# Kernel tuning notes

Hardware: AMD Instinct MI355X
Metric: run time of the kernel (lower is better)

The kernel has to match this reference:

```python
import math
import jax, jax.numpy as jnp
import numpy as np

B, N, D, H, PQ, PV = 2, 2048, 256, 8, 4, 8
HD = D // H
OUT_IN = D + H * PV * 3 + H  # 256 + 192 + 8 = 456


def setup_inputs() -> dict:
    key = jax.random.key(0)
    ks = jax.random.split(key, 12)
    w = lambda k, shape: (jax.random.normal(k, shape, jnp.float32) * 0.02)
    return {
        "x": jax.random.normal(ks[0], (B, N, D), jnp.float32),
        "rotations": jax.random.normal(ks[1], (B, N, 3, 3), jnp.float32),
        "translations": jax.random.normal(ks[2], (B, N, 3), jnp.float32),
        "mask": jnp.ones((B, N), dtype=bool),
        "Wq": w(ks[3], (D, D)), "bq": jnp.zeros((D,), jnp.float32),
        "Wk": w(ks[4], (D, D)), "bk": jnp.zeros((D,), jnp.float32),
        "Wv": w(ks[5], (D, D)), "bv": jnp.zeros((D,), jnp.float32),
        "Wo": w(ks[6], (OUT_IN, D)), "bo": jnp.zeros((D,), jnp.float32),
        "head_weights": jnp.ones((H,), jnp.float32),
    }


def reference(x, rotations, translations, mask, Wq, bq, Wk, bk, Wv, bv, Wo, bo, head_weights):
    b, n, d = x.shape
    h = head_weights.shape[0]
    hd = d // h
    pv3 = Wo.shape[0] - d - h  # num_heads * num_value_points * 3

    q = (x @ Wq + bq).reshape(b, n, h, hd)
    k = (x @ Wk + bk).reshape(b, n, h, hd)
    v = (x @ Wv + bv).reshape(b, n, h, hd)

    # scalar attention logits [b,h,i,j]
    attn_scores = jnp.einsum("bihd,bjhd->bhij", q, k) / math.sqrt(hd)

    # point-distance bias from frame translations (rotated q/k/v points are
    # dead code in the original module and are omitted)
    diff = translations[:, :, None, :] - translations[:, None, :, :]  # [b,i,j,3]
    dist_sq = jnp.sum(diff * diff, axis=-1)                            # [b,i,j]
    point_attn = -0.5 * dist_sq[:, None, :, :]                         # [b,1,i,j]

    weights = jax.nn.softmax(head_weights)                             # [h]
    combined = attn_scores + point_attn * weights[None, :, None, None]
    combined = jnp.where(mask[:, None, None, :], combined, -1e9)
    attn_probs = jax.nn.softmax(combined, axis=-1)                     # [b,h,i,j]

    attn_output = jnp.einsum("bhij,bjhd->bihd", attn_probs, v).reshape(b, n, d)

    # translation-weighted points, brought back to local frame
    trans_weighted = jnp.einsum("bhij,bjc->bihc", attn_probs, translations)  # [b,i,h,3]
    trans_local = trans_weighted - translations[:, :, None, :]
    point_out = trans_local.reshape(b, n, h * 3)
    point_out = jnp.pad(point_out, ((0, 0), (0, 0), (0, pv3 - h * 3)))

    mean_dist = jnp.sqrt(jnp.mean(dist_sq, axis=-1, keepdims=True) + 1e-8)  # [b,n,1]
    pair_features = jnp.broadcast_to(mean_dist, (b, n, h))

    output = jnp.concatenate([attn_output, point_out, pair_features], axis=-1)
    return output @ Wo + bo
```

## Files before the change

### kernel.cpp

```cpp
#include <hip/hip_runtime.h>

typedef unsigned short u16;
typedef __attribute__((ext_vector_type(8))) short bf16x8;
typedef __attribute__((ext_vector_type(4))) float f32x4;
typedef __attribute__((ext_vector_type(16))) float f32x16;
typedef __attribute__((ext_vector_type(4))) unsigned u32x4;

#define NB 2
#define NSEQ 2048
#define DD 256
#define NH 8
#define HD 32
#define NTOK 4096
#define KF 288
#define NSPLIT 4
#define PS 36
#define TSTR 4096

#define SCL2E 0.25506973f
#define L2E 1.4426950408889634f

__device__ __forceinline__ u16 f2b(float f) {
  unsigned u = __builtin_bit_cast(unsigned, f);
  return (u16)((u + 0x7fffu + ((u >> 16) & 1u)) >> 16);
}

__device__ __forceinline__ unsigned cvt_pk_bf16(float lo, float hi) {
  unsigned r;
  asm("v_cvt_pk_bf16_f32 %0, %1, %2" : "=v"(r) : "v"(lo), "v"(hi));
  return r;
}

__device__ __forceinline__ void permlane32_swap(unsigned& a, unsigned& b) {
  asm volatile("v_permlane32_swap_b32 %0, %1" : "+v"(a), "+v"(b));
}

__device__ __forceinline__ f32x4 mfma16(bf16x8 a, bf16x8 b, f32x4 c) {
  return __builtin_amdgcn_mfma_f32_16x16x32_bf16(a, b, c, 0, 0, 0);
}
__device__ __forceinline__ f32x16 mfma32(bf16x8 a, bf16x8 b, f32x16 c) {
  return __builtin_amdgcn_mfma_f32_32x32x16_bf16(a, b, c, 0, 0, 0);
}

#define PB0 1024
#define PB1 (PB0 + 264)
#define PB2 (PB1 + 2)
#define PB3 (PB2 + 16)
__global__ __launch_bounds__(256) void prep(
    const float* __restrict__ x, const float* __restrict__ tr,
    const float* __restrict__ hw, const float* __restrict__ bq,
    const float* __restrict__ bk, const float* __restrict__ bv,
    const float* __restrict__ Wq, const float* __restrict__ Wk,
    const float* __restrict__ Wv, const float* __restrict__ Wo,
    u16* __restrict__ xb, u16* __restrict__ WqkvT, u16* __restrict__ WoPT,
    float4* __restrict__ t4, float4* __restrict__ bstat,
    float* __restrict__ b_all, float* __restrict__ wsoft) {
  __shared__ float lt[32][33];
  const int bid = blockIdx.x, t = threadIdx.x;
  if (bid < PB0) {
    const int i4 = bid * 256 + t;
    float4 v = *(const float4*)(x + (size_t)i4 * 4);
    ushort4 o;
    o.x = f2b(v.x); o.y = f2b(v.y); o.z = f2b(v.z); o.w = f2b(v.w);
    *(ushort4*)(xb + (size_t)i4 * 4) = o;
  } else if (bid < PB1) {
    const int bw = bid - PB0;
    const int r = t >> 3, c4 = (t & 7) * 4;
    if (bw < 192) {
      int mt = bw >> 3, kt = bw & 7;
      int m0 = mt * 32, k0 = kt * 32;
      const float* W = m0 < 256 ? Wq : (m0 < 512 ? Wk : Wv);
      const int mm = m0 & 255;
      float4 v = *(const float4*)(W + (size_t)(k0 + r) * 256 + mm + c4);
      lt[r][c4] = v.x; lt[r][c4 + 1] = v.y; lt[r][c4 + 2] = v.z; lt[r][c4 + 3] = v.w;
      __syncthreads();
      const float s = m0 < 256 ? SCL2E : 1.f;
      ushort4 o;
      o.x = f2b(lt[c4][r] * s); o.y = f2b(lt[c4 + 1][r] * s);
      o.z = f2b(lt[c4 + 2][r] * s); o.w = f2b(lt[c4 + 3][r] * s);
      *(ushort4*)(WqkvT + (size_t)(m0 + r) * 256 + k0 + c4) = o;
    } else {
      int q = bw - 192;
      int nt2 = q / 9, kt = q - nt2 * 9;
      int n0 = nt2 * 32, kk0 = kt * 32;
      int row = (kk0 + r) < 280 ? (kk0 + r) : (kk0 + r + 168);
      float4 v = *(const float4*)(Wo + (size_t)row * 256 + n0 + c4);
      lt[r][c4] = v.x; lt[r][c4 + 1] = v.y; lt[r][c4 + 2] = v.z; lt[r][c4 + 3] = v.w;
      __syncthreads();
      ushort4 o;
      o.x = f2b(lt[c4][r]); o.y = f2b(lt[c4 + 1][r]);
      o.z = f2b(lt[c4 + 2][r]); o.w = f2b(lt[c4 + 3][r]);
      *(ushort4*)(WoPT + (size_t)(n0 + r) * KF + kk0 + c4) = o;
    }
  } else if (bid < PB2) {
    const int b = bid - PB1;
    float sx = 0.f, sy = 0.f, sz = 0.f, s2 = 0.f;
    for (int j = t; j < NSEQ; j += 256) {
      float a = tr[(size_t)(b * NSEQ + j) * 3];
      float b2 = tr[(size_t)(b * NSEQ + j) * 3 + 1];
      float c = tr[(size_t)(b * NSEQ + j) * 3 + 2];
      sx += a; sy += b2; sz += c; s2 += a * a + b2 * b2 + c * c;
    }
#pragma unroll
    for (int off = 1; off < 64; off <<= 1) {
      sx += __shfl_xor(sx, off); sy += __shfl_xor(sy, off);
      sz += __shfl_xor(sz, off); s2 += __shfl_xor(s2, off);
    }
    __shared__ float4 red[4];
    if ((t & 63) == 0) red[t >> 6] = make_float4(sx, sy, sz, s2);
    __syncthreads();
    if (t == 0) {
      float4 a = red[0], b1 = red[1], c = red[2], d = red[3];
      bstat[b] = make_float4(a.x + b1.x + c.x + d.x, a.y + b1.y + c.y + d.y,
                             a.z + b1.z + c.z + d.z, a.w + b1.w + c.w + d.w);
    }
  } else if (bid < PB3) {
    const int j = (bid - PB2) * 256 + t;
    float a = tr[j * 3], b2 = tr[j * 3 + 1], c = tr[j * 3 + 2];
    t4[j] = make_float4(a, b2, c, a * a + b2 * b2 + c * c);
  } else {
    for (int i = t; i < 768; i += 256)
      b_all[i] = i < 256 ? bq[i] * SCL2E : i < 512 ? bk[i - 256] : bv[i - 512];
    if (t == 0) {
      float mx = hw[0];
      for (int i = 1; i < NH; i++) mx = fmaxf(mx, hw[i]);
      float e[NH], sum = 0.f;
      for (int i = 0; i < NH; i++) { e[i] = __expf(hw[i] - mx); sum += e[i]; }
      for (int i = 0; i < NH; i++) wsoft[i] = e[i] / sum;
    }
  }
}

template <int M, int K>
__global__ __launch_bounds__(256) void gemm_big(
    const u16* __restrict__ AT, const u16* __restrict__ BT,
    const float* __restrict__ bias, u16* __restrict__ out) {
  const int lane = threadIdx.x & 63, wv = threadIdx.x >> 6;
  const int il = lane & 15, g = lane >> 4;
  const int wm = wv >> 1, wn = wv & 1;
  const int mblk = blockIdx.y * 64 + wm * 32;
  const int nblk = blockIdx.x * 128 + wn * 64;
  f32x4 acc[2][4];
#pragma unroll
  for (int a = 0; a < 2; a++)
#pragma unroll
    for (int b = 0; b < 4; b++) acc[a][b] = (f32x4)(0.f);
  const u16* Abase = AT + (size_t)(mblk + il) * K + 8 * g;
  const u16* Bbase = BT + (size_t)(nblk + il) * K + 8 * g;
#pragma unroll
  for (int kk = 0; kk < K; kk += 32) {
    bf16x8 aF[2], bF[4];
#pragma unroll
    for (int mt = 0; mt < 2; mt++)
      aF[mt] = *(const bf16x8*)(Abase + (size_t)mt * 16 * K + kk);
#pragma unroll
    for (int nt = 0; nt < 4; nt++)
      bF[nt] = *(const bf16x8*)(Bbase + (size_t)nt * 16 * K + kk);
#pragma unroll
    for (int mt = 0; mt < 2; mt++)
#pragma unroll
      for (int nt = 0; nt < 4; nt++)
        acc[mt][nt] = mfma16(aF[mt], bF[nt], acc[mt][nt]);
  }
#pragma unroll
  for (int nt = 0; nt < 4; nt++) {
    const int n_g = nblk + nt * 16 + il;
#pragma unroll
    for (int mt = 0; mt < 2; mt++) {
      const int m0 = mblk + mt * 16 + 4 * g;
      f32x4 v = acc[mt][nt];
      const float4 bb = *(const float4*)(bias + m0);
      v[0] += bb.x; v[1] += bb.y; v[2] += bb.z; v[3] += bb.w;
      ushort4 u;
      u.x = f2b(v[0]); u.y = f2b(v[1]); u.z = f2b(v[2]); u.w = f2b(v[3]);
      *(ushort4*)(out + (size_t)n_g * M + m0) = u;
    }
  }
}

template <int M, int K>
__global__ __launch_bounds__(256) void gemm_out(
    const u16* __restrict__ AT, const u16* __restrict__ BT,
    const float* __restrict__ bias, float* __restrict__ outv) {
  const int lane = threadIdx.x & 63, wv = threadIdx.x >> 6;
  const int il = lane & 15, g = lane >> 4;
  const int wm = wv >> 1, wn = wv & 1;
  const int mblk = blockIdx.y * 32 + wm * 16;
  const int nblk = blockIdx.x * 64 + wn * 32;
  f32x4 acc[2];
  acc[0] = (f32x4)(0.f);
  acc[1] = (f32x4)(0.f);
  const u16* Abase = AT + (size_t)(mblk + il) * K + 8 * g;
  const u16* Bbase = BT + (size_t)(nblk + il) * K + 8 * g;
#pragma unroll
  for (int kk = 0; kk < K; kk += 32) {
    bf16x8 aF = *(const bf16x8*)(Abase + kk);
    bf16x8 bF0 = *(const bf16x8*)(Bbase + kk);
    bf16x8 bF1 = *(const bf16x8*)(Bbase + (size_t)16 * K + kk);
    acc[0] = mfma16(aF, bF0, acc[0]);
    acc[1] = mfma16(aF, bF1, acc[1]);
  }
#pragma unroll
  for (int nt = 0; nt < 2; nt++) {
    const int n_g = nblk + nt * 16 + il;
    const int m0 = mblk + 4 * g;
    f32x4 v = acc[nt];
    const float4 bb = *(const float4*)(bias + m0);
    v[0] += bb.x; v[1] += bb.y; v[2] += bb.z; v[3] += bb.w;
    *(float4*)(outv + (size_t)n_g * M + m0) = make_float4(v[0], v[1], v[2], v[3]);
  }
}

__global__ __launch_bounds__(256) void repack(
    const u16* __restrict__ QKV, const float* __restrict__ tr,
    u16* __restrict__ TLB) {
  __shared__ u16 ldsV[32][33];
  const int jt = blockIdx.x, h = blockIdx.y, b = blockIdx.z;
  const int t = threadIdx.x;
  u16* tile = TLB + ((size_t)((b * NH + h) * 64 + jt)) * TSTR;
  if (t < 128) {
    const int rr = t & 31, dd = t >> 5;
    const int tok = b * NSEQ + jt * 32 + rr;
    bf16x8 kv = *(const bf16x8*)(QKV + (size_t)tok * 768 + 256 + h * 32 + dd * 8);
    *(bf16x8*)(tile + (size_t)(dd * 32 + rr) * 8) = kv;
    if (t < 64) {
      const int c = t >> 1, hi = t & 1;
      const int tok2 = b * NSEQ + jt * 32 + c;
      float a = tr[tok2 * 3], b2 = tr[tok2 * 3 + 1], cz = tr[tok2 * 3 + 2];
      u16 ov[8];
#pragma unroll
      for (int e = 0; e < 8; e++) {
        int ea = hi * 8 + e;
        float v = ea == 0 ? a : ea == 1 ? b2 : ea == 2 ? cz
                  : ea == 3 ? (a * a + b2 * b2 + cz * cz) : ea == 4 ? 1.f : 0.f;
        ov[e] = f2b(v);
      }
      *(bf16x8*)(tile + 3072 + c * 16 + hi * 8) = *(bf16x8*)ov;
    }
  } else {
    const int u = t - 128;
    const int rr = u & 31, dd = u >> 5;
    const int tok = b * NSEQ + jt * 32 + rr;
    bf16x8 vv = *(const bf16x8*)(QKV + (size_t)tok * 768 + 512 + h * 32 + dd * 8);
#pragma unroll
    for (int e = 0; e < 8; e++) ldsV[rr][dd * 8 + e] = (u16)vv[e];
  }
  __syncthreads();
  if (t >= 128) {
    const int u = t - 128;
    const int c2 = u & 31, sub = u >> 5;
    const int jb2 = (sub >> 1) * 16 + (sub & 1) * 8;
    u16 ov[8];
#pragma unroll
    for (int e = 0; e < 8; e++) ov[e] = ldsV[jb2 + e][c2];
    *(bf16x8*)(tile + 1024 + (size_t)u * 8) = *(bf16x8*)ov;
  } else {
    const int c2 = t & 31, sub = t >> 5;
    const int jb2 = (sub >> 1) * 16 + (sub & 1) * 8;
    u16 ov[8];
#pragma unroll
    for (int e = 0; e < 8; e++) {
      float v = 0.f;
      if (c2 == 0) v = 1.f;
      else if (c2 < 4) v = tr[(size_t)(b * NSEQ + jt * 32 + jb2 + e) * 3 + c2 - 1];
      ov[e] = f2b(v);
    }
    *(bf16x8*)(tile + 2048 + (size_t)t * 8) = *(bf16x8*)ov;
  }
}

__global__ __launch_bounds__(256, 4) void attn_kernel(
    const u16* __restrict__ QKV, const u16* __restrict__ TLB,
    const float4* __restrict__ t4, const float* __restrict__ wsoft,
    float* __restrict__ part) {
  __shared__ __align__(16) u16 tlb[2][4096];
  const int tid = threadIdx.x;
  const int lane = tid & 63, wv = tid >> 6;
  const int c = lane & 31, hi = lane >> 5;
  const int bh = blockIdx.y, b = bh >> 3, h = bh & 7;
  const int s = blockIdx.z;
  const int qb = blockIdx.x * 128 + wv * 32;
  const int iglob = b * NSEQ + qb + c;

  const u16* qptr = QKV + (size_t)iglob * 768 + h * HD + 8 * hi;
  const bf16x8 qf0 = *(const bf16x8*)qptr;
  const bf16x8 qf1 = *(const bf16x8*)(qptr + 16);
  const float4 ti = t4[iglob];
  const float w = wsoft[h];
  const float WD = w * L2E, NH2 = -0.5f * WD;
  u32x4 vw = (u32x4)(0u);
  if (hi == 0) {
    vw[0] = cvt_pk_bf16(WD * ti.x, WD * ti.y);
    vw[1] = cvt_pk_bf16(WD * ti.z, NH2);
    vw[2] = cvt_pk_bf16(NH2 * ti.w, 0.f);
  }
  const bf16x8 vf = __builtin_bit_cast(bf16x8, vw);

  f32x16 o = (f32x16)(0.f), aacc = (f32x16)(0.f);
  const u16* tbase = TLB + (size_t)bh * 64 * TSTR;
  const int jt0 = s * 16;
  const int fo = hi * 256 + c * 8;

  bf16x8 g0, g1;
  {
    const u16* src = tbase + (size_t)jt0 * TSTR;
    g0 = *(const bf16x8*)(src + tid * 8);
    if (tid < 192) g1 = *(const bf16x8*)(src + 2048 + tid * 8);
    *(bf16x8*)(&tlb[0][tid * 8]) = g0;
    if (tid < 192) *(bf16x8*)(&tlb[0][2048 + tid * 8]) = g1;
  }
  __syncthreads();

#pragma unroll 2
  for (int t = 0; t < 16; ++t) {
    if (t < 15) {
      const u16* src = tbase + (size_t)(jt0 + t + 1) * TSTR;
      g0 = *(const bf16x8*)(src + tid * 8);
      if (tid < 192) g1 = *(const bf16x8*)(src + 2048 + tid * 8);
    }
    const u16* L = &tlb[t & 1][0];
    bf16x8 k0 = *(const bf16x8*)(L + fo);
    bf16x8 k1 = *(const bf16x8*)(L + 512 + fo);
    bf16x8 v0 = *(const bf16x8*)(L + 1024 + fo);
    bf16x8 v1 = *(const bf16x8*)(L + 1536 + fo);
    bf16x8 a0 = *(const bf16x8*)(L + 2048 + fo);
    bf16x8 a1 = *(const bf16x8*)(L + 2560 + fo);
    bf16x8 uf = *(const bf16x8*)(L + 3072 + c * 16 + hi * 8);
    __builtin_amdgcn_s_setprio(1);
    f32x16 sa = mfma32(uf, vf, (f32x16)(0.f));
    sa = mfma32(k0, qf0, sa);
    sa = mfma32(k1, qf1, sa);
    float p[16];
#pragma unroll
    for (int r = 0; r < 16; r++) p[r] = exp2f(sa[r]);
    unsigned x0 = cvt_pk_bf16(p[0], p[1]), y0 = cvt_pk_bf16(p[4], p[5]);
    unsigned z0 = cvt_pk_bf16(p[2], p[3]), w0 = cvt_pk_bf16(p[6], p[7]);
    permlane32_swap(x0, y0);
    permlane32_swap(z0, w0);
    unsigned x1 = cvt_pk_bf16(p[8], p[9]), y1 = cvt_pk_bf16(p[12], p[13]);
    unsigned z1 = cvt_pk_bf16(p[10], p[11]), w1 = cvt_pk_bf16(p[14], p[15]);
    permlane32_swap(x1, y1);
    permlane32_swap(z1, w1);
    bf16x8 pa0 = __builtin_bit_cast(bf16x8, (u32x4){x0, z0, y0, w0});
    bf16x8 pa1 = __builtin_bit_cast(bf16x8, (u32x4){x1, z1, y1, w1});
    o = mfma32(pa0, v0, o);
    o = mfma32(pa1, v1, o);
    aacc = mfma32(pa0, a0, aacc);
    aacc = mfma32(pa1, a1, aacc);
    __builtin_amdgcn_s_setprio(0);
    if (t < 15) {
      u16* D = &tlb[(t + 1) & 1][0];
      *(bf16x8*)(D + tid * 8) = g0;
      if (tid < 192) *(bf16x8*)(D + 2048 + tid * 8) = g1;
    }
    __syncthreads();
  }

  float* pbase = part + ((size_t)(s * 16 + bh) * NSEQ + qb) * PS;
#pragma unroll
  for (int r = 0; r < 16; r++) {
    const int irow = (r & 3) + 8 * (r >> 2) + 4 * hi;
    float* pr = pbase + (size_t)irow * PS;
    pr[c] = o[r];
    if (c < 4) pr[32 + c] = aacc[r];
  }
}

__global__ __launch_bounds__(256) void combine_kernel(
    const float* __restrict__ part, const float4* __restrict__ t4,
    const float4* __restrict__ bstat, u16* __restrict__ feats) {
  const int lane = threadIdx.x & 63;
  const int gw = blockIdx.x * 4 + (threadIdx.x >> 6);
  const int bh = gw >> 11, i = gw & 2047;
  const int b = bh >> 3, h = bh & 7;
  const int tok = b * NSEQ + i;
  const float* p0 = part + ((size_t)bh * NSEQ + i) * PS;
  const size_t SS = (size_t)16 * NSEQ * PS;
  float v = 0.f;
  if (lane < PS) v = p0[lane] + p0[SS + lane] + p0[2 * SS + lane] + p0[3 * SS + lane];
  float ls = __shfl(v, 32);
  float inv = 1.f / ls;
  u16* fr = feats + (size_t)tok * KF;
  if (lane < 32) {
    fr[h * HD + lane] = f2b(v * inv);
  } else if (lane >= 33 && lane < 36) {
    int cc = lane - 33;
    float tc = cc == 0 ? t4[tok].x : (cc == 1 ? t4[tok].y : t4[tok].z);
    fr[256 + h * 3 + cc] = f2b(fmaf(v, inv, -tc));
  } else if (lane == 36 && h == 0) {
    float4 t = t4[tok];
    float4 st = bstat[b];
    float sumd = (float)NSEQ * t.w + st.w -
                 2.f * (t.x * st.x + t.y * st.y + t.z * st.z);
    float md = sqrtf(sumd * (1.f / (float)NSEQ) + 1e-8f);
    u16 mb = f2b(md);
    for (int cc = 0; cc < 8; cc++) fr[280 + cc] = mb;
  }
}

extern "C" void kernel_launch(void* const* d_in, const int* in_sizes, int n_in,
                              void* d_out, int out_size, void* d_ws, size_t ws_size,
                              hipStream_t stream) {
  (void)in_sizes; (void)n_in; (void)out_size; (void)ws_size;
  const float* x  = (const float*)d_in[0];
  const float* tr = (const float*)d_in[2];
  const float* Wq = (const float*)d_in[4];
  const float* bq = (const float*)d_in[5];
  const float* Wk = (const float*)d_in[6];
  const float* bk = (const float*)d_in[7];
  const float* Wv = (const float*)d_in[8];
  const float* bv = (const float*)d_in[9];
  const float* Wo = (const float*)d_in[10];
  const float* bo = (const float*)d_in[11];
  const float* hw = (const float*)d_in[12];
  float* out = (float*)d_out;

  char* p = (char*)d_ws;
  auto alloc = [&](size_t n) { char* r = p; p += (n + 255) & ~(size_t)255; return r; };
  u16* xb      = (u16*)alloc((size_t)NTOK * DD * 2);
  u16* WqkvT   = (u16*)alloc((size_t)768 * DD * 2);
  u16* WoPT    = (u16*)alloc((size_t)DD * KF * 2);
  float4* t4   = (float4*)alloc((size_t)NTOK * 16);
  float* b_all = (float*)alloc(768 * 4);
  float* ws    = (float*)alloc(256);
  float4* bst  = (float4*)alloc(256);
  u16* QKV     = (u16*)alloc((size_t)NTOK * 768 * 2);
  u16* TLB     = (u16*)alloc((size_t)NB * NH * 64 * TSTR * 2);
  u16* feats   = (u16*)alloc((size_t)NTOK * KF * 2);
  float* part  = (float*)alloc((size_t)NSPLIT * 16 * NSEQ * PS * 4);

  prep<<<PB3 + 1, 256, 0, stream>>>(x, tr, hw, bq, bk, bv, Wq, Wk, Wv, Wo, xb,
                                    WqkvT, WoPT, t4, bst, b_all, ws);
  gemm_big<768, DD><<<dim3(32, 12), 256, 0, stream>>>(WqkvT, xb, b_all, QKV);
  repack<<<dim3(64, NH, NB), 256, 0, stream>>>(QKV, tr, TLB);
  attn_kernel<<<dim3(NSEQ / 128, NB * NH, NSPLIT), 256, 0, stream>>>(
      QKV, TLB, t4, ws, part);
  combine_kernel<<<8192, 256, 0, stream>>>(part, t4, bst, feats);
  gemm_out<DD, KF><<<dim3(64, 8), 256, 0, stream>>>(WoPT, feats, bo, out);
}
```

Before: 142.5 us.

## Fuse combine into output GEMM and share per-batch translation tiles across heads

```diff
diff --git a/kernel.cpp b/kernel.cpp
--- a/kernel.cpp
+++ b/kernel.cpp
@@ -10,12 +10,18 @@
 #define NSEQ 2048
 #define DD 256
 #define NH 8
-#define HD 32
 #define NTOK 4096
 #define KF 288
+#define KFP 296
 #define NSPLIT 4
 #define PS 36
-#define TSTR 4096
+#define TSTR 2048
+
+#define L_V 1024
+#define L_A 2048
+#define L_U 3072
+#define L_ZP 3328
+#define L_STR 3344
 
 #define SCL2E 0.25506973f
 #define L2E 1.4426950408889634f
@@ -42,10 +48,13 @@
   return __builtin_amdgcn_mfma_f32_32x32x16_bf16(a, b, c, 0, 0, 0);
 }
 
-#define PB0 1024
-#define PB1 (PB0 + 264)
-#define PB2 (PB1 + 2)
-#define PB3 (PB2 + 16)
+#define PB_XB 1024
+#define PB_WT (PB_XB + 264)
+#define PB_BS (PB_WT + 2)
+#define PB_T4 (PB_BS + 16)
+#define PB_UC (PB_T4 + 128)
+#define PB_AC (PB_UC + 64)
+#define PB_N  (PB_AC + 1)
 __global__ __launch_bounds__(256) void prep(
     const float* __restrict__ x, const float* __restrict__ tr,
     const float* __restrict__ hw, const float* __restrict__ bq,
@@ -54,17 +63,19 @@
     const float* __restrict__ Wv, const float* __restrict__ Wo,
     u16* __restrict__ xb, u16* __restrict__ WqkvT, u16* __restrict__ WoPT,
     float4* __restrict__ t4, float4* __restrict__ bstat,
+    u16* __restrict__ UC, u16* __restrict__ AC,
     float* __restrict__ b_all, float* __restrict__ wsoft) {
   __shared__ float lt[32][33];
+  __shared__ float4 red[4];
   const int bid = blockIdx.x, t = threadIdx.x;
-  if (bid < PB0) {
+  if (bid < PB_XB) {
     const int i4 = bid * 256 + t;
     float4 v = *(const float4*)(x + (size_t)i4 * 4);
     ushort4 o;
     o.x = f2b(v.x); o.y = f2b(v.y); o.z = f2b(v.z); o.w = f2b(v.w);
     *(ushort4*)(xb + (size_t)i4 * 4) = o;
-  } else if (bid < PB1) {
-    const int bw = bid - PB0;
+  } else if (bid < PB_WT) {
+    const int bw = bid - PB_XB;
     const int r = t >> 3, c4 = (t & 7) * 4;
     if (bw < 192) {
       int mt = bw >> 3, kt = bw & 7;
@@ -92,8 +103,8 @@
       o.z = f2b(lt[c4 + 2][r]); o.w = f2b(lt[c4 + 3][r]);
       *(ushort4*)(WoPT + (size_t)(n0 + r) * KF + kk0 + c4) = o;
     }
-  } else if (bid < PB2) {
-    const int b = bid - PB1;
+  } else if (bid < PB_BS) {
+    const int b = bid - PB_WT;
     float sx = 0.f, sy = 0.f, sz = 0.f, s2 = 0.f;
     for (int j = t; j < NSEQ; j += 256) {
       float a = tr[(size_t)(b * NSEQ + j) * 3];
@@ -106,7 +117,6 @@
       sx += __shfl_xor(sx, off); sy += __shfl_xor(sy, off);
       sz += __shfl_xor(sz, off); s2 += __shfl_xor(s2, off);
     }
-    __shared__ float4 red[4];
     if ((t & 63) == 0) red[t >> 6] = make_float4(sx, sy, sz, s2);
     __syncthreads();
     if (t == 0) {
@@ -114,10 +124,29 @@
       bstat[b] = make_float4(a.x + b1.x + c.x + d.x, a.y + b1.y + c.y + d.y,
                              a.z + b1.z + c.z + d.z, a.w + b1.w + c.w + d.w);
     }
-  } else if (bid < PB3) {
-    const int j = (bid - PB2) * 256 + t;
+  } else if (bid < PB_T4) {
+    const int j = (bid - PB_BS) * 256 + t;
     float a = tr[j * 3], b2 = tr[j * 3 + 1], c = tr[j * 3 + 2];
     t4[j] = make_float4(a, b2, c, a * a + b2 * b2 + c * c);
+  } else if (bid < PB_UC) {
+    const int id = (bid - PB_T4) * 256 + t;
+    const int b = id >> 14, jt = (id >> 8) & 63, c = (id >> 3) & 31, e = id & 7;
+    const int tok = b * NSEQ + jt * 32 + c;
+    float v = 0.f;
+    if (e < 3) v = tr[(size_t)tok * 3 + e];
+    else if (e == 3) {
+      float a = tr[(size_t)tok * 3], b2 = tr[(size_t)tok * 3 + 1],
+            cz = tr[(size_t)tok * 3 + 2];
+      v = a * a + b2 * b2 + cz * cz;
+    } else if (e == 4) v = 1.f;
+    UC[id] = f2b(v);
+  } else if (bid < PB_AC) {
+    const int id = (bid - PB_UC) * 256 + t;
+    const int b = id >> 13, jt = (id >> 7) & 63, sub = (id >> 5) & 3,
+              cch = (id >> 3) & 3, e = id & 7;
+    const int j = jt * 32 + (sub >> 1) * 16 + (sub & 1) * 8 + e;
+    float v = cch == 0 ? 1.f : tr[(size_t)(b * NSEQ + j) * 3 + cch - 1];
+    AC[id] = f2b(v);
   } else {
     for (int i = t; i < 768; i += 256)
       b_all[i] = i < 256 ? bq[i] * SCL2E : i < 512 ? bk[i - 256] : bv[i - 512];
@@ -178,42 +207,8 @@
   }
 }
 
-template <int M, int K>
-__global__ __launch_bounds__(256) void gemm_out(
-    const u16* __restrict__ AT, const u16* __restrict__ BT,
-    const float* __restrict__ bias, float* __restrict__ outv) {
-  const int lane = threadIdx.x & 63, wv = threadIdx.x >> 6;
-  const int il = lane & 15, g = lane >> 4;
-  const int wm = wv >> 1, wn = wv & 1;
-  const int mblk = blockIdx.y * 32 + wm * 16;
-  const int nblk = blockIdx.x * 64 + wn * 32;
-  f32x4 acc[2];
-  acc[0] = (f32x4)(0.f);
-  acc[1] = (f32x4)(0.f);
-  const u16* Abase = AT + (size_t)(mblk + il) * K + 8 * g;
-  const u16* Bbase = BT + (size_t)(nblk + il) * K + 8 * g;
-#pragma unroll
-  for (int kk = 0; kk < K; kk += 32) {
-    bf16x8 aF = *(const bf16x8*)(Abase + kk);
-    bf16x8 bF0 = *(const bf16x8*)(Bbase + kk);
-    bf16x8 bF1 = *(const bf16x8*)(Bbase + (size_t)16 * K + kk);
-    acc[0] = mfma16(aF, bF0, acc[0]);
-    acc[1] = mfma16(aF, bF1, acc[1]);
-  }
-#pragma unroll
-  for (int nt = 0; nt < 2; nt++) {
-    const int n_g = nblk + nt * 16 + il;
-    const int m0 = mblk + 4 * g;
-    f32x4 v = acc[nt];
-    const float4 bb = *(const float4*)(bias + m0);
-    v[0] += bb.x; v[1] += bb.y; v[2] += bb.z; v[3] += bb.w;
-    *(float4*)(outv + (size_t)n_g * M + m0) = make_float4(v[0], v[1], v[2], v[3]);
-  }
-}
-
 __global__ __launch_bounds__(256) void repack(
-    const u16* __restrict__ QKV, const float* __restrict__ tr,
-    u16* __restrict__ TLB) {
+    const u16* __restrict__ QKV, u16* __restrict__ TLB) {
   __shared__ u16 ldsV[32][33];
   const int jt = blockIdx.x, h = blockIdx.y, b = blockIdx.z;
   const int t = threadIdx.x;
@@ -223,20 +218,6 @@
     const int tok = b * NSEQ + jt * 32 + rr;
     bf16x8 kv = *(const bf16x8*)(QKV + (size_t)tok * 768 + 256 + h * 32 + dd * 8);
     *(bf16x8*)(tile + (size_t)(dd * 32 + rr) * 8) = kv;
-    if (t < 64) {
-      const int c = t >> 1, hi = t & 1;
-      const int tok2 = b * NSEQ + jt * 32 + c;
-      float a = tr[tok2 * 3], b2 = tr[tok2 * 3 + 1], cz = tr[tok2 * 3 + 2];
-      u16 ov[8];
-#pragma unroll
-      for (int e = 0; e < 8; e++) {
-        int ea = hi * 8 + e;
-        float v = ea == 0 ? a : ea == 1 ? b2 : ea == 2 ? cz
-                  : ea == 3 ? (a * a + b2 * b2 + cz * cz) : ea == 4 ? 1.f : 0.f;
-        ov[e] = f2b(v);
-      }
-      *(bf16x8*)(tile + 3072 + c * 16 + hi * 8) = *(bf16x8*)ov;
-    }
   } else {
     const int u = t - 128;
     const int rr = u & 31, dd = u >> 5;
@@ -254,35 +235,27 @@
 #pragma unroll
     for (int e = 0; e < 8; e++) ov[e] = ldsV[jb2 + e][c2];
     *(bf16x8*)(tile + 1024 + (size_t)u * 8) = *(bf16x8*)ov;
-  } else {
-    const int c2 = t & 31, sub = t >> 5;
-    const int jb2 = (sub >> 1) * 16 + (sub & 1) * 8;
-    u16 ov[8];
-#pragma unroll
-    for (int e = 0; e < 8; e++) {
-      float v = 0.f;
-      if (c2 == 0) v = 1.f;
-      else if (c2 < 4) v = tr[(size_t)(b * NSEQ + jt * 32 + jb2 + e) * 3 + c2 - 1];
-      ov[e] = f2b(v);
-    }
-    *(bf16x8*)(tile + 2048 + (size_t)t * 8) = *(bf16x8*)ov;
   }
 }
 
 __global__ __launch_bounds__(256, 4) void attn_kernel(
     const u16* __restrict__ QKV, const u16* __restrict__ TLB,
+    const u16* __restrict__ UC, const u16* __restrict__ AC,
     const float4* __restrict__ t4, const float* __restrict__ wsoft,
     float* __restrict__ part) {
-  __shared__ __align__(16) u16 tlb[2][4096];
+  __shared__ __align__(16) u16 lds[2 * L_STR];
   const int tid = threadIdx.x;
   const int lane = tid & 63, wv = tid >> 6;
   const int c = lane & 31, hi = lane >> 5;
-  const int bh = blockIdx.y, b = bh >> 3, h = bh & 7;
-  const int s = blockIdx.z;
-  const int qb = blockIdx.x * 128 + wv * 32;
+  const int bid = blockIdx.x;
+  const int idx = bid >> 3;
+  const int c2 = (bid & 7) * 8 + (idx >> 4);
+  const int bh = c2 >> 2, s = c2 & 3;
+  const int b = bh >> 3, h = bh & 7;
+  const int qb = (idx & 15) * 128 + wv * 32;
   const int iglob = b * NSEQ + qb + c;
 
-  const u16* qptr = QKV + (size_t)iglob * 768 + h * HD + 8 * hi;
+  const u16* qptr = QKV + (size_t)iglob * 768 + h * 32 + 8 * hi;
   const bf16x8 qf0 = *(const bf16x8*)qptr;
   const bf16x8 qf1 = *(const bf16x8*)(qptr + 16);
   const float4 ti = t4[iglob];
@@ -297,35 +270,45 @@
   const bf16x8 vf = __builtin_bit_cast(bf16x8, vw);
 
   f32x16 o = (f32x16)(0.f), aacc = (f32x16)(0.f);
-  const u16* tbase = TLB + (size_t)bh * 64 * TSTR;
   const int jt0 = s * 16;
+  const u16* tK = TLB + ((size_t)bh * 64 + jt0) * TSTR;
+  const u16* tA = AC + ((size_t)b * 64 + jt0) * 128;
+  const u16* tU = UC + ((size_t)b * 64 + jt0) * 256;
   const int fo = hi * 256 + c * 8;
 
-  bf16x8 g0, g1;
   {
-    const u16* src = tbase + (size_t)jt0 * TSTR;
-    g0 = *(const bf16x8*)(src + tid * 8);
-    if (tid < 192) g1 = *(const bf16x8*)(src + 2048 + tid * 8);
-    *(bf16x8*)(&tlb[0][tid * 8]) = g0;
-    if (tid < 192) *(bf16x8*)(&tlb[0][2048 + tid * 8]) = g1;
+    unsigned* zz = (unsigned*)lds;
+    for (int i = tid; i < 1296; i += 256) {
+      int k = (i < 648) ? (L_A / 2 + i) : (L_STR / 2 + L_A / 2 + i - 648);
+      zz[k] = 0;
+    }
   }
   __syncthreads();
-
-#pragma unroll 2
+  bf16x8 gkv = *(const bf16x8*)(tK + (size_t)tid * 8);
+  bf16x8 ga, gu;
+  if (tid < 16) ga = *(const bf16x8*)(tA + tid * 8);
+  else if (tid < 48) gu = *(const bf16x8*)(tU + (tid - 16) * 8);
+  *(bf16x8*)(lds + tid * 8) = gkv;
+  if (tid < 16) *(bf16x8*)(lds + L_A + (tid >> 2) * 256 + (tid & 3) * 8) = ga;
+  else if (tid < 48) *(bf16x8*)(lds + L_U + (tid - 16) * 8) = gu;
+  __syncthreads();
+
+#pragma unroll 1
   for (int t = 0; t < 16; ++t) {
     if (t < 15) {
-      const u16* src = tbase + (size_t)(jt0 + t + 1) * TSTR;
-      g0 = *(const bf16x8*)(src + tid * 8);
-      if (tid < 192) g1 = *(const bf16x8*)(src + 2048 + tid * 8);
-    }
-    const u16* L = &tlb[t & 1][0];
+      gkv = *(const bf16x8*)(tK + (size_t)(t + 1) * TSTR + tid * 8);
+      if (tid < 16) ga = *(const bf16x8*)(tA + (size_t)(t + 1) * 128 + tid * 8);
+      else if (tid < 48)
+        gu = *(const bf16x8*)(tU + (size_t)(t + 1) * 256 + (tid - 16) * 8);
+    }
+    const u16* L = lds + (t & 1) * L_STR;
     bf16x8 k0 = *(const bf16x8*)(L + fo);
     bf16x8 k1 = *(const bf16x8*)(L + 512 + fo);
-    bf16x8 v0 = *(const bf16x8*)(L + 1024 + fo);
-    bf16x8 v1 = *(const bf16x8*)(L + 1536 + fo);
-    bf16x8 a0 = *(const bf16x8*)(L + 2048 + fo);
-    bf16x8 a1 = *(const bf16x8*)(L + 2560 + fo);
-    bf16x8 uf = *(const bf16x8*)(L + 3072 + c * 16 + hi * 8);
+    bf16x8 v0 = *(const bf16x8*)(L + L_V + fo);
+    bf16x8 v1 = *(const bf16x8*)(L + L_V + 512 + fo);
+    bf16x8 a0 = *(const bf16x8*)(L + L_A + fo);
+    bf16x8 a1 = *(const bf16x8*)(L + L_A + 512 + fo);
+    bf16x8 uf = *(const bf16x8*)(hi ? (L + L_ZP) : (L + L_U + c * 8));
     __builtin_amdgcn_s_setprio(1);
     f32x16 sa = mfma32(uf, vf, (f32x16)(0.f));
     sa = mfma32(k0, qf0, sa);
@@ -349,9 +332,10 @@
     aacc = mfma32(pa1, a1, aacc);
     __builtin_amdgcn_s_setprio(0);
     if (t < 15) {
-      u16* D = &tlb[(t + 1) & 1][0];
-      *(bf16x8*)(D + tid * 8) = g0;
-      if (tid < 192) *(bf16x8*)(D + 2048 + tid * 8) = g1;
+      u16* D = lds + ((t + 1) & 1) * L_STR;
+      *(bf16x8*)(D + tid * 8) = gkv;
+      if (tid < 16) *(bf16x8*)(D + L_A + (tid >> 2) * 256 + (tid & 3) * 8) = ga;
+      else if (tid < 48) *(bf16x8*)(D + L_U + (tid - 16) * 8) = gu;
     }
     __syncthreads();
   }
@@ -366,35 +350,74 @@
   }
 }
 
-__global__ __launch_bounds__(256) void combine_kernel(
-    const float* __restrict__ part, const float4* __restrict__ t4,
-    const float4* __restrict__ bstat, u16* __restrict__ feats) {
-  const int lane = threadIdx.x & 63;
-  const int gw = blockIdx.x * 4 + (threadIdx.x >> 6);
-  const int bh = gw >> 11, i = gw & 2047;
-  const int b = bh >> 3, h = bh & 7;
-  const int tok = b * NSEQ + i;
-  const float* p0 = part + ((size_t)bh * NSEQ + i) * PS;
+__global__ __launch_bounds__(256) void outk(
+    const float* __restrict__ part, const u16* __restrict__ WoPT,
+    const float* __restrict__ bo, const float4* __restrict__ t4,
+    const float4* __restrict__ bstat, const float* __restrict__ tr,
+    float* __restrict__ out) {
+  __shared__ __align__(16) u16 feats[16][KFP];
+  __shared__ float invl[16][8];
+  const int t = threadIdx.x;
+  const int tok0 = blockIdx.x * 16;
+  const int b = tok0 >> 11;
+  const int i0 = tok0 & 2047;
   const size_t SS = (size_t)16 * NSEQ * PS;
-  float v = 0.f;
-  if (lane < PS) v = p0[lane] + p0[SS + lane] + p0[2 * SS + lane] + p0[3 * SS + lane];
-  float ls = __shfl(v, 32);
-  float inv = 1.f / ls;
-  u16* fr = feats + (size_t)tok * KF;
-  if (lane < 32) {
-    fr[h * HD + lane] = f2b(v * inv);
-  } else if (lane >= 33 && lane < 36) {
-    int cc = lane - 33;
-    float tc = cc == 0 ? t4[tok].x : (cc == 1 ? t4[tok].y : t4[tok].z);
-    fr[256 + h * 3 + cc] = f2b(fmaf(v, inv, -tc));
-  } else if (lane == 36 && h == 0) {
-    float4 t = t4[tok];
+  if (t < 128) {
+    const int r = t >> 3, hh = t & 7;
+    const float* p = part + ((size_t)(b * 8 + hh) * NSEQ + i0 + r) * PS + 32;
+    invl[r][hh] = 1.f / (p[0] + p[SS] + p[2 * SS] + p[3 * SS]);
+  }
+  __syncthreads();
+#pragma unroll
+  for (int ii = 0; ii < 16; ++ii) {
+    const int id = t + 256 * ii;
+    const int r = id >> 8, cc = id & 255;
+    const float* p =
+        part + ((size_t)(b * 8 + (cc >> 5)) * NSEQ + i0 + r) * PS + (cc & 31);
+    float v = p[0] + p[SS] + p[2 * SS] + p[3 * SS];
+    feats[r][cc] = f2b(v * invl[r][cc >> 5]);
+  }
+  for (int id = t; id < 384; id += 256) {
+    const int r = id / 24, cc = id - r * 24;
+    const int comp = cc % 3, hh = cc / 3;
+    const float* p =
+        part + ((size_t)(b * 8 + hh) * NSEQ + i0 + r) * PS + 33 + comp;
+    float v = p[0] + p[SS] + p[2 * SS] + p[3 * SS];
+    feats[r][256 + cc] =
+        f2b(v * invl[r][hh] - tr[(size_t)(tok0 + r) * 3 + comp]);
+  }
+  if (t < 128) {
+    const int r = t >> 3;
+    float4 tt = t4[tok0 + r];
     float4 st = bstat[b];
-    float sumd = (float)NSEQ * t.w + st.w -
-                 2.f * (t.x * st.x + t.y * st.y + t.z * st.z);
-    float md = sqrtf(sumd * (1.f / (float)NSEQ) + 1e-8f);
-    u16 mb = f2b(md);
-    for (int cc = 0; cc < 8; cc++) fr[280 + cc] = mb;
+    float sumd = (float)NSEQ * tt.w + st.w -
+                 2.f * (tt.x * st.x + tt.y * st.y + tt.z * st.z);
+    feats[r][280 + (t & 7)] = f2b(sqrtf(sumd * (1.f / (float)NSEQ) + 1e-8f));
+  }
+  __syncthreads();
+  const int lane = t & 63, wv = t >> 6;
+  const int il = lane & 15, g = lane >> 4;
+  f32x4 acc[4];
+#pragma unroll
+  for (int mt = 0; mt < 4; mt++) acc[mt] = (f32x4)(0.f);
+  const u16* Ab = WoPT + (size_t)(wv * 64 + il) * KF + 8 * g;
+#pragma unroll
+  for (int kk = 0; kk < KF; kk += 32) {
+    bf16x8 bF = *(const bf16x8*)(&feats[il][kk + 8 * g]);
+#pragma unroll
+    for (int mt = 0; mt < 4; mt++) {
+      bf16x8 aF = *(const bf16x8*)(Ab + (size_t)mt * 16 * KF + kk);
+      acc[mt] = mfma16(aF, bF, acc[mt]);
+    }
+  }
+  const int n_g = tok0 + il;
+#pragma unroll
+  for (int mt = 0; mt < 4; mt++) {
+    const int m0 = wv * 64 + mt * 16 + 4 * g;
+    f32x4 v = acc[mt];
+    const float4 bb = *(const float4*)(bo + m0);
+    v[0] += bb.x; v[1] += bb.y; v[2] += bb.z; v[3] += bb.w;
+    *(float4*)(out + (size_t)n_g * DD + m0) = make_float4(v[0], v[1], v[2], v[3]);
   }
 }
 
@@ -424,17 +447,16 @@
   float* b_all = (float*)alloc(768 * 4);
   float* ws    = (float*)alloc(256);
   float4* bst  = (float4*)alloc(256);
+  u16* UC      = (u16*)alloc((size_t)NB * 64 * 256 * 2);
+  u16* AC      = (u16*)alloc((size_t)NB * 64 * 128 * 2);
   u16* QKV     = (u16*)alloc((size_t)NTOK * 768 * 2);
   u16* TLB     = (u16*)alloc((size_t)NB * NH * 64 * TSTR * 2);
-  u16* feats   = (u16*)alloc((size_t)NTOK * KF * 2);
   float* part  = (float*)alloc((size_t)NSPLIT * 16 * NSEQ * PS * 4);
 
-  prep<<<PB3 + 1, 256, 0, stream>>>(x, tr, hw, bq, bk, bv, Wq, Wk, Wv, Wo, xb,
-                                    WqkvT, WoPT, t4, bst, b_all, ws);
+  prep<<<PB_N, 256, 0, stream>>>(x, tr, hw, bq, bk, bv, Wq, Wk, Wv, Wo, xb,
+                                 WqkvT, WoPT, t4, bst, UC, AC, b_all, ws);
   gemm_big<768, DD><<<dim3(32, 12), 256, 0, stream>>>(WqkvT, xb, b_all, QKV);
-  repack<<<dim3(64, NH, NB), 256, 0, stream>>>(QKV, tr, TLB);
-  attn_kernel<<<dim3(NSEQ / 128, NB * NH, NSPLIT), 256, 0, stream>>>(
-      QKV, TLB, t4, ws, part);
-  combine_kernel<<<8192, 256, 0, stream>>>(part, t4, bst, feats);
-  gemm_out<DD, KF><<<dim3(64, 8), 256, 0, stream>>>(WoPT, feats, bo, out);
-}
+  repack<<<dim3(64, NH, NB), 256, 0, stream>>>(QKV, TLB);
+  attn_kernel<<<1024, 256, 0, stream>>>(QKV, TLB, UC, AC, t4, ws, part);
+  outk<<<256, 256, 0, stream>>>(part, WoPT, bo, t4, bst, tr, out);
+}
```

After: 138.8 us. 2.6% less time.
